# Optimization experiments

Measured on AMD Instinct MI355X. Metric: run time of the kernel, lower is better.

Reference implementation:

```python
import jax, jax.numpy as jnp
import numpy as np

EPS = 1e-5

def _batchnorm(x, gamma, beta):
    # BatchNorm1d in training mode: stats over the point (N) dimension, biased var
    mean = x.mean(axis=0)
    var = ((x - mean) ** 2).mean(axis=0)
    return (x - mean) * jax.lax.rsqrt(var + EPS) * gamma + beta

def setup_inputs() -> dict:
    key = jax.random.key(0)
    ks = jax.random.split(key, 6)
    N, C_in, K, B = 262144, 3, 64, 16
    return {
        "feats": jax.random.normal(ks[0], (N, C_in), dtype=jnp.float32),
        "batch_idx": jax.random.randint(ks[1], (N,), 0, B, dtype=jnp.int32),
        "W1": jax.random.normal(ks[2], (128, C_in), dtype=jnp.float32) * 0.1,
        "gamma1": jnp.ones((128,), jnp.float32),
        "beta1": jnp.zeros((128,), jnp.float32),
        "W2": jax.random.normal(ks[3], (64, 256), dtype=jnp.float32) * 0.05,
        "gamma2": jnp.ones((64,), jnp.float32),
        "beta2": jnp.zeros((64,), jnp.float32),
        "W3": jax.random.normal(ks[4], (K, 64), dtype=jnp.float32) * 0.1,
        "b3": jnp.zeros((K,), jnp.float32),
        "num_batches": B,
    }

def reference(feats, batch_idx, W1, gamma1, beta1, W2, gamma2, beta2, W3, b3, num_batches):
    # conv1 (1x1 conv == linear, no bias) + bn1
    x = _batchnorm(feats @ W1.T, gamma1, beta1)          # [N,128]
    # per-batch global max pooling, broadcast back to points
    seg_max = jax.ops.segment_max(x, batch_idx, num_segments=num_batches)  # [B,128]
    x = jnp.concatenate([x, seg_max[batch_idx]], axis=1)  # [N,256]
    # conv2 + bn2 + relu
    x = jax.nn.relu(_batchnorm(x @ W2.T, gamma2, beta2))  # [N,64]
    # conv3 (with bias)
    return x @ W3.T + b3                                   # [N,k]
```

## Files before the change

kernel.cpp:

```cpp
#include <hip/hip_runtime.h>
#include <hip/hip_bf16.h>

#define EPS 1e-5f
#define NPTS 262144
#define NB 16

typedef __attribute__((ext_vector_type(8))) short bf16x8;
typedef __attribute__((ext_vector_type(4))) float f32x4;

#define WS_E    0
#define WS_T    192
#define WS_W3   1216
#define WS_MAXF 3264
#define WS_PMOM 5312
#define WS_SCRM 6480
#define WS_SMAX 43856

__device__ inline float decodeu(unsigned u){
  unsigned bits = (u & 0x80000000u) ? (u ^ 0x80000000u) : ~u;
  return __uint_as_float(bits);
}
__device__ inline unsigned f2bf(float f){
  unsigned u = __float_as_uint(f);
  return (u + 0x7FFFu + ((u>>16)&1u)) >> 16;
}
__device__ inline unsigned pack2bf(float lo, float hi){
  return (f2bf(hi)<<16) | (f2bf(lo) & 0xFFFFu);
}
__device__ inline unsigned ordu(float v){
  unsigned bits = __float_as_uint(v);
  return bits ^ (unsigned)(((int)bits>>31) | (int)0x80000000);
}

__global__ __launch_bounds__(1024) void kAC(const float* __restrict__ feats,
                                            const int* __restrict__ bidx,
                                            const float* __restrict__ W1,
                                            const float* __restrict__ g1,
                                            float* __restrict__ wsf) {
  __shared__ unsigned lmax[NB*128];
  __shared__ __align__(16) float4 sfeat[512];
  __shared__ float hist[4][NB*4];
  __shared__ float red[8*9];
  __shared__ unsigned cnt[NB], base[NB];
  int tid = threadIdx.x;
  int lane = tid&63, wv = tid>>6;
  for (int i=tid;i<NB*128;i+=1024) lmax[i]=0u;
  if (tid < 4*NB*4) ((float*)hist)[tid]=0.f;
  if (tid < NB) cnt[tid]=0u;
  __syncthreads();
  bool stager = (tid < 512);
  float f0=0.f, f1=0.f, f2=0.f; int b=0; unsigned pos=0;
  if (stager){
    int p = blockIdx.x*512 + tid;
    f0=feats[3*p]; f1=feats[3*p+1]; f2=feats[3*p+2];
    b = bidx[p];
    int hrep = wv >> 1;
    atomicAdd(&hist[hrep][b*4+0],f0);
    atomicAdd(&hist[hrep][b*4+1],f1);
    atomicAdd(&hist[hrep][b*4+2],f2);
    atomicAdd(&hist[hrep][b*4+3],1.0f);
    pos = atomicAdd(&cnt[b], 1u);
  }
  if (wv < 8){
    float acc[9]={f0,f1,f2,f0*f0,f0*f1,f0*f2,f1*f1,f1*f2,f2*f2};
    #pragma unroll
    for (int k=0;k<9;k++){
      float v=acc[k];
      v+=__shfl_down(v,32); v+=__shfl_down(v,16); v+=__shfl_down(v,8);
      v+=__shfl_down(v,4);  v+=__shfl_down(v,2);  v+=__shfl_down(v,1);
      if (lane==0) red[wv*9+k]=v;
    }
  }
  __syncthreads();
  if (tid==0){
    unsigned s=0;
    #pragma unroll
    for (int q=0;q<NB;q++){ base[q]=s; s+=cnt[q]; }
  }
  __syncthreads();
  if (stager) sfeat[base[b]+pos] = make_float4(f0,f1,f2,__int_as_float(b));
  __syncthreads();
  int c0 = lane, c1 = lane+64;
  float sg0 = (g1[c0]>=0.f)?1.f:-1.f;
  float sg1 = (g1[c1]>=0.f)?1.f:-1.f;
  float w00=W1[3*c0]*sg0, w01=W1[3*c0+1]*sg0, w02=W1[3*c0+2]*sg0;
  float w10=W1[3*c1]*sg1, w11=W1[3*c1+1]*sg1, w12=W1[3*c1+2]*sg1;
  const float4* sp = &sfeat[wv*32];
  int bcur = -1; float mm0=0.f, mm1=0.f;
  #pragma unroll 8
  for (int k=0;k<32;k++){
    float4 f = sp[k];
    float v0 = fmaf(f.z,w02,fmaf(f.y,w01,f.x*w00));
    float v1 = fmaf(f.z,w12,fmaf(f.y,w11,f.x*w10));
    int b2 = __builtin_amdgcn_readfirstlane(__float_as_int(f.w));
    if (b2 != bcur){
      if (bcur >= 0){
        atomicMax(&lmax[bcur*128+c0], ordu(mm0));
        atomicMax(&lmax[bcur*128+c1], ordu(mm1));
      }
      bcur = b2; mm0 = v0; mm1 = v1;
    } else {
      mm0 = fmaxf(mm0,v0); mm1 = fmaxf(mm1,v1);
    }
  }
  atomicMax(&lmax[bcur*128+c0], ordu(mm0));
  atomicMax(&lmax[bcur*128+c1], ordu(mm1));
  __syncthreads();
  float* scrM = wsf + WS_SCRM + blockIdx.x*73;
  if (tid<9){
    float s=0;
    #pragma unroll
    for (int q=0;q<8;q++) s += red[q*9+tid];
    scrM[tid]=s;
  }
  if (tid>=64 && tid<128){
    int i = tid-64;
    scrM[9+i] = hist[0][i]+hist[1][i]+hist[2][i]+hist[3][i];
  }
  unsigned* spo = (unsigned*)wsf + WS_SMAX + (size_t)blockIdx.x*2048;
  for (int i=tid;i<2048;i+=1024) spo[i]=lmax[i];
}

__global__ __launch_bounds__(512) void kMx(const float* __restrict__ W3,
                                           float* __restrict__ wsf){
  __shared__ unsigned red[32][16];
  __shared__ float mred[2][73];
  int tid = threadIdx.x, blk = blockIdx.x;
  int g = tid >> 4;
  int e = blk*16 + (tid & 15);
  const unsigned* smax = (const unsigned*)wsf + WS_SMAX;
  unsigned m = 0;
  #pragma unroll 8
  for (int k=g*16; k<g*16+16; k++){
    unsigned t = smax[(size_t)k*2048 + e];
    m = t>m ? t : m;
  }
  red[g][tid&15] = m;
  if (blk < 16 && tid < 146){
    int h = (tid >= 73) ? 1 : 0, mm = tid - 73*h;
    float s = 0; const float* sm0 = wsf + WS_SCRM;
    int k0 = blk*32 + h*16;
    #pragma unroll 4
    for (int k=k0; k<k0+16; k++) s += sm0[k*73 + mm];
    mred[h][mm] = s;
  }
  if (blk >= 32 && blk < 34){
    int q = (blk-32)*512 + tid;
    float4 v = ((const float4*)W3)[q];
    unsigned* w3u = (unsigned*)wsf + WS_W3;
    w3u[2*q]   = pack2bf(v.x, v.y);
    w3u[2*q+1] = pack2bf(v.z, v.w);
  }
  __syncthreads();
  if (tid < 16){
    unsigned u = red[0][tid];
    #pragma unroll
    for (int q=1;q<32;q++){ unsigned t=red[q][tid]; u = t>u?t:u; }
    ((unsigned*)wsf)[WS_MAXF + blk*16 + tid] = u;
  }
  if (blk < 16 && tid < 73)
    wsf[WS_PMOM + blk*73 + tid] = mred[0][tid] + mred[1][tid];
}

__global__ __launch_bounds__(128) void kB2(const float* __restrict__ W1,
    const float* __restrict__ g1, const float* __restrict__ b1,
    const float* __restrict__ W2, const float* __restrict__ g2,
    const float* __restrict__ b2, float* __restrict__ wsf){
  __shared__ float spm[16*73];
  __shared__ float smom[80];
  __shared__ float dred[2][20];
  __shared__ float sfin[20];
  __shared__ float pY[16], pYY[16], hbs[16];
  __shared__ float s2t2[2];
  int tid = threadIdx.x, c = blockIdx.x;
  int lane = tid & 63, wv = tid >> 6;
  for (int i=tid;i<16*73;i+=128) spm[i] = wsf[WS_PMOM + i];
  int j = tid;
  float w2f = W2[c*256 + j];
  float w2b = W2[c*256 + 128 + j];
  float w10 = W1[3*j], w11 = W1[3*j+1], w12 = W1[3*j+2];
  float g1j = g1[j], b1j = b1[j];
  unsigned um[16];
  { const unsigned* mf = (const unsigned*)wsf + WS_MAXF;
    #pragma unroll
    for (int b=0;b<16;b++) um[b] = mf[b*128 + j];
  }
  __syncthreads();
  if (tid < 73){
    float s = 0;
    #pragma unroll
    for (int g=0; g<16; g++) s += spm[g*73 + tid];
    smom[tid] = s;
  }
  __syncthreads();
  const float invN = 1.0f/NPTS;
  float mean = (w10*smom[0]+w11*smom[1]+w12*smom[2])*invN;
  float ex2 = (w10*w10*smom[3]+w11*w11*smom[6]+w12*w12*smom[8]
             + 2.f*(w10*w11*smom[4]+w10*w12*smom[5]+w11*w12*smom[7]))*invN;
  float var = ex2 - mean*mean;
  float sc = g1j*rsqrtf(var+EPS);
  float sh = b1j - mean*sc;
  float asc = fabsf(sc);
  float p[20];
  p[0] = w2f*(sc*w10); p[1] = w2f*(sc*w11); p[2] = w2f*(sc*w12); p[3] = w2f*sh;
  #pragma unroll
  for (int b=0;b<16;b++) p[4+b] = w2b * fmaf(asc, decodeu(um[b]), sh);
  #pragma unroll
  for (int k=0;k<20;k++){
    float v = p[k];
    v+=__shfl_down(v,32); v+=__shfl_down(v,16); v+=__shfl_down(v,8);
    v+=__shfl_down(v,4);  v+=__shfl_down(v,2);  v+=__shfl_down(v,1);
    if (lane==0) dred[wv][k] = v;
  }
  __syncthreads();
  if (tid < 20) sfin[tid] = dred[0][tid] + dred[1][tid];
  __syncthreads();
  if (tid < 16){
    int b = tid;
    float e0=sfin[0],e1=sfin[1],e2=sfin[2],gc=sfin[3];
    float nb = smom[9+b*4+3];
    float hb = gc + sfin[4+b];
    float eS1b = e0*smom[9+b*4]+e1*smom[9+b*4+1]+e2*smom[9+b*4+2];
    hbs[b]=hb; pY[b]=nb*hb; pYY[b]=2.f*hb*eS1b+nb*hb*hb;
  }
  __syncthreads();
  if (tid == 0){
    float e0=sfin[0],e1=sfin[1],e2=sfin[2];
    float sumY = e0*smom[0]+e1*smom[1]+e2*smom[2];
    float sumYY = e0*e0*smom[3]+e1*e1*smom[6]+e2*e2*smom[8]
               + 2.f*(e0*e1*smom[4]+e0*e2*smom[5]+e1*e2*smom[7]);
    #pragma unroll
    for (int b=0;b<16;b++){ sumY += pY[b]; sumYY += pYY[b]; }
    float mean2 = sumY*invN;
    float var2 = sumYY*invN - mean2*mean2;
    float s2 = g2[c]*rsqrtf(var2+EPS);
    float t2 = b2[c] - mean2*s2;
    wsf[WS_E + c]      = e0*s2;
    wsf[WS_E + 64 + c] = e1*s2;
    wsf[WS_E + 128 + c]= e2*s2;
    s2t2[0]=s2; s2t2[1]=t2;
  }
  __syncthreads();
  if (tid < 16) wsf[WS_T + tid*64 + c] = hbs[tid]*s2t2[0] + s2t2[1];
}

__global__ __launch_bounds__(256, 4) void kF(const float* __restrict__ feats,
                                             const int* __restrict__ bidx,
                                             const float* __restrict__ wsf,
                                             const float* __restrict__ b3,
                                             float* __restrict__ out) {
  __shared__ __align__(16) unsigned char SB[37888];
  unsigned* zbuf = (unsigned*)SB;
  float* Tl = (float*)(SB + 32768);
  float* sEg = (float*)(SB + 37120);
  int tid = threadIdx.x;
  for (int i=tid;i<NB*64;i+=256) Tl[(i>>6)*68 + (i&63)] = wsf[WS_T + i];
  if (tid < 192) sEg[tid] = wsf[WS_E + tid];
  int lane = tid & 63, wv = tid >> 6;
  int col = lane & 15, kgrp = lane >> 4;
  const ushort* w3b = (const ushort*)((const unsigned*)wsf + WS_W3);
  bf16x8 bfr[4][2];
  #pragma unroll
  for (int n=0;n<4;n++)
    #pragma unroll
    for (int kk=0;kk<2;kk++)
      bfr[n][kk] = *(const bf16x8*)(w3b + (n*16+col)*64 + kk*32 + kgrp*8);
  float bias[4];
  #pragma unroll
  for (int n=0;n<4;n++) bias[n] = b3[n*16+col];
  const f32x4* e04 = (const f32x4*)(sEg);
  const f32x4* e14 = (const f32x4*)(sEg + 64);
  const f32x4* e24 = (const f32x4*)(sEg + 128);
  __syncthreads();
  int p0 = (blockIdx.x*4 + wv)*64;
  int p = p0 + lane;
  float f0 = feats[3*p], f1 = feats[3*p+1], f2 = feats[3*p+2];
  int b = bidx[p];
  const f32x4* tb4 = (const f32x4*)&Tl[b*68];
  unsigned rowbase = (unsigned)(wv*64+lane)*32;
  unsigned sw = (lane&7)<<2;
  #pragma unroll
  for (int j=0;j<8;j++){
    unsigned w[4];
    #pragma unroll
    for (int h=0;h<2;h++){
      int cq = j*2 + h;
      f32x4 e0 = e04[cq], e1 = e14[cq], e2 = e24[cq], tp = tb4[cq];
      float y0 = fmaf(e0[0],f0, fmaf(e1[0],f1, fmaf(e2[0],f2, tp[0])));
      float y1 = fmaf(e0[1],f0, fmaf(e1[1],f1, fmaf(e2[1],f2, tp[1])));
      float y2 = fmaf(e0[2],f0, fmaf(e1[2],f1, fmaf(e2[2],f2, tp[2])));
      float y3 = fmaf(e0[3],f0, fmaf(e1[3],f1, fmaf(e2[3],f2, tp[3])));
      w[h*2]   = pack2bf(fmaxf(y0,0.f), fmaxf(y1,0.f));
      w[h*2+1] = pack2bf(fmaxf(y2,0.f), fmaxf(y3,0.f));
    }
    uint4 ch; ch.x=w[0]; ch.y=w[1]; ch.z=w[2]; ch.w=w[3];
    *(uint4*)&zbuf[rowbase + (((unsigned)(j*4)) ^ sw)] = ch;
  }
  asm volatile("s_waitcnt lgkmcnt(0)" ::: "memory");
  __builtin_amdgcn_sched_barrier(0);
  bf16x8 af[4][2];
  #pragma unroll
  for (int m=0;m<4;m++){
    int row = m*16 + col;
    unsigned rb = (unsigned)(wv*64+row)*32;
    unsigned sw2 = (unsigned)(row&7)<<2;
    #pragma unroll
    for (int kk=0;kk<2;kk++){
      unsigned off = ((unsigned)(kk*16 + kgrp*4)) ^ sw2;
      af[m][kk] = *(const bf16x8*)&zbuf[rb + off];
    }
  }
  asm volatile("s_waitcnt lgkmcnt(0)" ::: "memory");
  __builtin_amdgcn_sched_barrier(0);
  float* fwave = (float*)(SB + wv*8192);
  #pragma unroll
  for (int half=0; half<2; half++){
    f32x4 acc[2][4];
    #pragma unroll
    for (int mi=0;mi<2;mi++)
      #pragma unroll
      for (int n=0;n<4;n++)
        acc[mi][n] = (f32x4){0.f,0.f,0.f,0.f};
    #pragma unroll
    for (int kk=0;kk<2;kk++)
      #pragma unroll
      for (int mi=0;mi<2;mi++)
        #pragma unroll
        for (int n=0;n<4;n++)
          acc[mi][n] = __builtin_amdgcn_mfma_f32_16x16x32_bf16(af[half*2+mi][kk], bfr[n][kk], acc[mi][n], 0,0,0);
    #pragma unroll
    for (int mi=0;mi<2;mi++){
      #pragma unroll
      for (int n=0;n<4;n++){
        #pragma unroll
        for (int r=0;r<4;r++)
          fwave[(mi*16 + kgrp*4 + r)*64 + n*16 + col] = acc[mi][n][r] + bias[n];
      }
    }
    asm volatile("s_waitcnt lgkmcnt(0)" ::: "memory");
    __builtin_amdgcn_sched_barrier(0);
    #pragma unroll
    for (int it=0; it<8; it++){
      int idx = it*64 + lane;
      int r = idx >> 4;
      int c4 = (idx & 15) * 4;
      f32x4 v = *(const f32x4*)&fwave[r*64 + c4];
      int orow = p0 + half*32 + r;
      __builtin_nontemporal_store(v, (f32x4*)&out[(size_t)orow*64 + c4]);
    }
    asm volatile("s_waitcnt lgkmcnt(0)" ::: "memory");
    __builtin_amdgcn_sched_barrier(0);
  }
}

extern "C" void kernel_launch(void* const* d_in, const int* in_sizes, int n_in,
                              void* d_out, int out_size, void* d_ws, size_t ws_size,
                              hipStream_t stream) {
  const float* feats = (const float*)d_in[0];
  const int*   bidx  = (const int*)d_in[1];
  const float* W1 = (const float*)d_in[2];
  const float* g1 = (const float*)d_in[3];
  const float* b1 = (const float*)d_in[4];
  const float* W2 = (const float*)d_in[5];
  const float* g2 = (const float*)d_in[6];
  const float* b2 = (const float*)d_in[7];
  const float* W3 = (const float*)d_in[8];
  const float* b3 = (const float*)d_in[9];
  float* wsf = (float*)d_ws;
  float* out = (float*)d_out;
  kAC<<<512, 1024, 0, stream>>>(feats, bidx, W1, g1, wsf);
  kMx<<<128, 512, 0, stream>>>(W3, wsf);
  kB2<<<64, 128, 0, stream>>>(W1, g1, b1, W2, g2, b2, wsf);
  kF<<<1024, 256, 0, stream>>>(feats, bidx, wsf, b3, out);
}
```

Baseline: 52.69 us.

## Swap MFMA operands to store output directly without LDS staging

Swaps the A/B operands of the final MFMA so each lane holds four consecutive output columns of one point. It can then write float4 results straight to global memory with nontemporal stores, skipping the LDS staging round trip and its waits. It also moves the per-point feats and batch-index global loads ahead of the shared-memory setup so their latency overlaps that setup. In exchange the direct stores are 16-byte pieces scattered over 16 rows per instruction, which may coalesce less well than the previous row-contiguous writes.

```diff
diff --git a/kernel.cpp b/kernel.cpp
--- a/kernel.cpp
+++ b/kernel.cpp
@@ -254,28 +254,28 @@
   float* Tl = (float*)(SB + 32768);
   float* sEg = (float*)(SB + 37120);
   int tid = threadIdx.x;
-  for (int i=tid;i<NB*64;i+=256) Tl[(i>>6)*68 + (i&63)] = wsf[WS_T + i];
-  if (tid < 192) sEg[tid] = wsf[WS_E + tid];
   int lane = tid & 63, wv = tid >> 6;
   int col = lane & 15, kgrp = lane >> 4;
-  const ushort* w3b = (const ushort*)((const unsigned*)wsf + WS_W3);
-  bf16x8 bfr[4][2];
-  #pragma unroll
-  for (int n=0;n<4;n++)
-    #pragma unroll
-    for (int kk=0;kk<2;kk++)
-      bfr[n][kk] = *(const bf16x8*)(w3b + (n*16+col)*64 + kk*32 + kgrp*8);
-  float bias[4];
-  #pragma unroll
-  for (int n=0;n<4;n++) bias[n] = b3[n*16+col];
-  const f32x4* e04 = (const f32x4*)(sEg);
-  const f32x4* e14 = (const f32x4*)(sEg + 64);
-  const f32x4* e24 = (const f32x4*)(sEg + 128);
-  __syncthreads();
   int p0 = (blockIdx.x*4 + wv)*64;
   int p = p0 + lane;
   float f0 = feats[3*p], f1 = feats[3*p+1], f2 = feats[3*p+2];
   int b = bidx[p];
+  for (int i=tid;i<NB*64;i+=256) Tl[(i>>6)*68 + (i&63)] = wsf[WS_T + i];
+  if (tid < 192) sEg[tid] = wsf[WS_E + tid];
+  const ushort* w3b = (const ushort*)((const unsigned*)wsf + WS_W3);
+  bf16x8 bfr[4][2];
+  #pragma unroll
+  for (int n=0;n<4;n++)
+    #pragma unroll
+    for (int kk=0;kk<2;kk++)
+      bfr[n][kk] = *(const bf16x8*)(w3b + (n*16+col)*64 + kk*32 + kgrp*8);
+  f32x4 bias4[4];
+  #pragma unroll
+  for (int n=0;n<4;n++) bias4[n] = *(const f32x4*)&b3[n*16 + kgrp*4];
+  const f32x4* e04 = (const f32x4*)(sEg);
+  const f32x4* e14 = (const f32x4*)(sEg + 64);
+  const f32x4* e24 = (const f32x4*)(sEg + 128);
+  __syncthreads();
   const f32x4* tb4 = (const f32x4*)&Tl[b*68];
   unsigned rowbase = (unsigned)(wv*64+lane)*32;
   unsigned sw = (lane&7)<<2;
@@ -312,44 +312,22 @@
   }
   asm volatile("s_waitcnt lgkmcnt(0)" ::: "memory");
   __builtin_amdgcn_sched_barrier(0);
-  float* fwave = (float*)(SB + wv*8192);
-  #pragma unroll
-  for (int half=0; half<2; half++){
-    f32x4 acc[2][4];
-    #pragma unroll
-    for (int mi=0;mi<2;mi++)
+  #pragma unroll
+  for (int m=0;m<4;m++){
+    f32x4 acc[4];
+    #pragma unroll
+    for (int n=0;n<4;n++) acc[n] = (f32x4){0.f,0.f,0.f,0.f};
+    #pragma unroll
+    for (int kk=0;kk<2;kk++)
       #pragma unroll
       for (int n=0;n<4;n++)
-        acc[mi][n] = (f32x4){0.f,0.f,0.f,0.f};
-    #pragma unroll
-    for (int kk=0;kk<2;kk++)
-      #pragma unroll
-      for (int mi=0;mi<2;mi++)
-        #pragma unroll
-        for (int n=0;n<4;n++)
-          acc[mi][n] = __builtin_amdgcn_mfma_f32_16x16x32_bf16(af[half*2+mi][kk], bfr[n][kk], acc[mi][n], 0,0,0);
-    #pragma unroll
-    for (int mi=0;mi<2;mi++){
-      #pragma unroll
-      for (int n=0;n<4;n++){
-        #pragma unroll
-        for (int r=0;r<4;r++)
-          fwave[(mi*16 + kgrp*4 + r)*64 + n*16 + col] = acc[mi][n][r] + bias[n];
-      }
-    }
-    asm volatile("s_waitcnt lgkmcnt(0)" ::: "memory");
-    __builtin_amdgcn_sched_barrier(0);
-    #pragma unroll
-    for (int it=0; it<8; it++){
-      int idx = it*64 + lane;
-      int r = idx >> 4;
-      int c4 = (idx & 15) * 4;
-      f32x4 v = *(const f32x4*)&fwave[r*64 + c4];
-      int orow = p0 + half*32 + r;
-      __builtin_nontemporal_store(v, (f32x4*)&out[(size_t)orow*64 + c4]);
-    }
-    asm volatile("s_waitcnt lgkmcnt(0)" ::: "memory");
-    __builtin_amdgcn_sched_barrier(0);
+        acc[n] = __builtin_amdgcn_mfma_f32_16x16x32_bf16(bfr[n][kk], af[m][kk], acc[n], 0,0,0);
+    int prow = p0 + m*16 + col;
+    #pragma unroll
+    for (int n=0;n<4;n++){
+      f32x4 v = acc[n] + bias4[n];
+      __builtin_nontemporal_store(v, (f32x4*)&out[(size_t)prow*64 + n*16 + kgrp*4]);
+    }
   }
 }
 
```

Measured after the change: 58.14 us. 10.4% more time.
